# Optimization experiments

Measured on AMD Instinct MI355X. Metric: run time of the kernel, lower is better.

The kernel has to match this reference:

```python
import jax, jax.numpy as jnp
import numpy as np
from jax import lax

FMAP = 64          # feature map H=W
STRIDE = 16
TILE = 16
IMG = 1024         # image H=W (image_shape[1]==image_shape[2])
PRE_NMS = 1000
POST_NMS = 300
NMS_THR = 0.7
RATIOS = np.array([0.5, 1.0, 2.0])
SCALES = np.array([8.0, 16.0, 32.0])


def _make_anchors():
    # meshgrid order (x, y, ratio, scale) with 'ij' indexing, then reshape(-1, 4)
    gx, gy, gr, gs = np.meshgrid(np.arange(FMAP), np.arange(FMAP),
                                 np.arange(len(RATIOS)), np.arange(len(SCALES)),
                                 indexing='ij')
    half_w = 0.5 * TILE * SCALES[gs] * np.sqrt(RATIOS[gr])
    half_h = 0.5 * TILE * SCALES[gs] * np.sqrt(1.0 / RATIOS[gr])
    cx = (gx + 0.5) * STRIDE
    cy = (gy + 0.5) * STRIDE
    z = np.stack([cx - half_w, cy - half_h, cx + half_w, cy + half_h], axis=-1)
    return jnp.asarray(z.reshape(-1, 4).astype(np.float32))  # (H*W*A, 4)


def setup_inputs() -> dict:
    key = jax.random.key(0)
    ks = jax.random.split(key, 6)
    B, Cin, F, A = 8, 256, 256, 9
    inputs = jax.random.normal(ks[0], (B, Cin, FMAP, FMAP), jnp.float32)
    bboxes = jax.random.uniform(ks[1], (B, 16, 4), jnp.float32) * IMG  # unused in inference path
    w_conv = jax.random.normal(ks[2], (F, Cin, 3, 3), jnp.float32) * 0.02
    b_conv = jnp.zeros((F,), jnp.float32)
    w_clf = jax.random.normal(ks[3], (2 * A, F, 1, 1), jnp.float32) * 0.02
    b_clf = jnp.zeros((2 * A,), jnp.float32)
    w_reg = jax.random.normal(ks[4], (4 * A, F, 1, 1), jnp.float32) * 0.02
    b_reg = jnp.zeros((4 * A,), jnp.float32)
    anchors = _make_anchors()
    return {"inputs": inputs, "bboxes": bboxes, "anchors": anchors,
            "w_conv": w_conv, "b_conv": b_conv,
            "w_clf": w_clf, "b_clf": b_clf,
            "w_reg": w_reg, "b_reg": b_reg}


def _conv(x, w, b):
    y = lax.conv_general_dilated(x, w, (1, 1), 'SAME',
                                 dimension_numbers=('NCHW', 'OIHW', 'NCHW'))
    return y + b[None, :, None, None]


def _nms_rois(boxes, batch_idx):
    # boxes: (PRE_NMS, 4), sorted by score descending. Greedy NMS.
    n = boxes.shape[0]
    lb = jnp.maximum(boxes[:, None, :2], boxes[None, :, :2])
    ub = jnp.minimum(boxes[:, None, 2:], boxes[None, :, 2:])
    inter = jnp.prod(jnp.clip(ub - lb, 0.0), axis=-1)              # (n, n)
    area = jnp.prod(boxes[:, 2:] - boxes[:, :2], axis=-1)          # (n,)
    iou = inter / (area[:, None] + area[None, :] - inter)
    idxs = jnp.arange(n)

    def body(i, keep):
        sup = (iou[i] > NMS_THR) & keep[i] & (idxs > i)
        return keep & ~sup

    keep = lax.fori_loop(0, n, body, jnp.ones((n,), bool))
    # compact kept boxes (in score order) into the first slots; OOB scatter drops
    pos = jnp.where(keep, jnp.cumsum(keep) - 1, n + POST_NMS)
    rois = jnp.zeros((POST_NMS, 5), boxes.dtype).at[:, 0].set(batch_idx.astype(boxes.dtype))
    rois = rois.at[pos, 1:].set(boxes, mode='drop')
    return rois


def reference(inputs, bboxes, anchors, w_conv, b_conv, w_clf, b_clf, w_reg, b_reg):
    B, _, H, W = inputs.shape
    x = jax.nn.relu(_conv(inputs, w_conv, b_conv))                  # (B, F, H, W)
    clf = _conv(x, w_clf, b_clf)                                    # (B, 2A, H, W)
    A = clf.shape[1] // 2
    prob = jax.nn.softmax(clf.reshape(B, 2, A, H, W), axis=1)
    scores = prob[:, 1].transpose(0, 2, 3, 1).reshape(B, -1)        # (B, H*W*A)
    reg = _conv(x, w_reg, b_reg).transpose(0, 2, 3, 1).reshape(B, -1, 4)
    # decode anchors with deltas
    sizes = anchors[:, 2:] - anchors[:, :2]                          # (N, 2)
    centers = 0.5 * (anchors[:, 2:] + anchors[:, :2])
    pred_centers = reg[..., :2] * sizes + centers
    pred_sizes = jnp.exp(reg[..., 2:]) * sizes
    props = jnp.concatenate([pred_centers - 0.5 * pred_sizes,
                             pred_centers + 0.5 * pred_sizes], axis=-1)
    lim = jnp.asarray([IMG - 1, IMG - 1, IMG - 1, IMG - 1], props.dtype)
    props = jnp.clip(props, 0.0, lim)
    # pre-NMS top-k by score
    _, top_idx = lax.top_k(scores, PRE_NMS)
    top_props = jnp.take_along_axis(props, top_idx[..., None], axis=1)  # (B, PRE, 4)
    rois = jax.vmap(_nms_rois)(top_props, jnp.arange(B))            # (B, POST, 5)
    return rois
```

## Files before the change

### kernel.cpp

```cpp
#include <hip/hip_runtime.h>

typedef unsigned long long ULL;
typedef double v4d __attribute__((ext_vector_type(4)));


__device__ __forceinline__ ULL fkey64(double f) {
    ULL u = (ULL)__double_as_longlong(f);
    return (u & 0x8000000000000000ull) ? ~u : (u | 0x8000000000000000ull);
}

__global__ void prep_all(const float* __restrict__ wconv,
                         const float* __restrict__ wclf, const float* __restrict__ bclf,
                         double* __restrict__ wmf,
                         double* __restrict__ wdiff, double* __restrict__ bdiff) {
    int blk = blockIdx.x;
    if (blk < 2304) {
        int e = blk * 256 + threadIdx.x;
        int co = e & 63;
        int r = e >> 6;
        int cil = r & 3;
        int r2 = r >> 2;
        int tap = r2 % 9;
        int r3 = r2 / 9;
        int cg = r3 & 3;
        int cc = r3 >> 2;
        int ci = cc * 4 + cil;
        int gco = cg * 64 + co;
        wmf[e] = (double)wconv[(gco * 256 + ci) * 9 + tap];
    } else {
        int a = blk - 2304;
        int c = threadIdx.x;
        wdiff[a * 256 + c] = (double)wclf[(9 + a) * 256 + c] - (double)wclf[a * 256 + c];
        if (c == 0) bdiff[a] = (double)bclf[9 + a] - (double)bclf[a];
    }
}

__global__ __launch_bounds__(256)
__attribute__((amdgpu_waves_per_eu(4, 4)))
void conv3x3_mfma_f64(
    const float* __restrict__ xin, const double* __restrict__ wmf,
    const float* __restrict__ bias, double* __restrict__ y)
{
    __shared__ double wlds[2304];
    __shared__ float  xs[864];

    const int t = threadIdx.x;
    const int blk = blockIdx.x;
    const int b = blk >> 8;
    const int h = (blk >> 2) & 63;
    const int cg = blk & 3;
    const int lane = t & 63;
    const int wid = t >> 6;
    const int arow = lane & 15;
    const int kq = lane >> 4;

    int x_ld[4], x_go[4];
#pragma unroll
    for (int i = 0; i < 4; i++) {
        int e = t + i * 256;
        x_ld[i] = -1; x_go[i] = -1;
        if (e < 792) {
            int cil = e / 198; int rem = e - cil * 198;
            int row = rem / 66; int c = rem - row * 66;
            int hh = h - 1 + row; int col = c - 1;
            x_ld[i] = cil * 216 + row * 72 + c;
            if (hh >= 0 && hh < 64 && col >= 0 && col < 64)
                x_go[i] = cil * 4096 + hh * 64 + col;
        }
    }

    const float* xb = xin + (size_t)b * 1048576;
    const double* wsrc = wmf + (size_t)cg * 2304;

    v4d pz = {0.0, 0.0, 0.0, 0.0};
    v4d prow = __builtin_amdgcn_mfma_f64_16x16x4f64((double)arow, 1.0, pz, 0, 0, 0);
    v4d pcol = __builtin_amdgcn_mfma_f64_16x16x4f64(1.0, (double)arow, pz, 0, 0, 0);
    int rmap[4], cmap[4];
#pragma unroll
    for (int g = 0; g < 4; g++) {
        rmap[g] = (int)(prow[g] * 0.25 + 0.5);
        cmap[g] = (int)(pcol[g] * 0.25 + 0.5);
    }

    float xreg[4];
    double wreg[9];
#pragma unroll
    for (int i = 0; i < 4; i++)
        xreg[i] = (x_ld[i] >= 0 && x_go[i] >= 0) ? xb[x_go[i]] : 0.f;
#pragma unroll
    for (int i = 0; i < 9; i++) wreg[i] = wsrc[t + i * 256];

    v4d acc[4];
#pragma unroll
    for (int nt = 0; nt < 4; nt++) acc[nt] = (v4d){0.0, 0.0, 0.0, 0.0};

    for (int cc = 0; cc < 64; ++cc) {
        __syncthreads();
#pragma unroll
        for (int i = 0; i < 4; i++) if (x_ld[i] >= 0) xs[x_ld[i]] = xreg[i];
#pragma unroll
        for (int i = 0; i < 9; i++) wlds[t + i * 256] = wreg[i];
        __syncthreads();

        if (cc < 63) {
#pragma unroll
            for (int i = 0; i < 4; i++)
                xreg[i] = (x_ld[i] >= 0 && x_go[i] >= 0) ? xb[(cc + 1) * 16384 + x_go[i]] : 0.f;
#pragma unroll
            for (int i = 0; i < 9; i++) wreg[i] = wsrc[(size_t)(cc + 1) * 9216 + t + i * 256];
        }

        const float* xsp = xs + kq * 216 + wid * 16 + arow;
        const double* wsp = wlds + kq * 64 + arow;
#pragma unroll
        for (int kh = 0; kh < 3; kh++) {
#pragma unroll
            for (int kw = 0; kw < 3; kw++) {
                const int tap = kh * 3 + kw;
                double a = (double)xsp[kh * 72 + kw];
#pragma unroll
                for (int nt = 0; nt < 4; nt++)
                    acc[nt] = __builtin_amdgcn_mfma_f64_16x16x4f64(
                        a, wsp[tap * 256 + nt * 16], acc[nt], 0, 0, 0);
            }
        }
    }

    const size_t pixbase = (size_t)(b * 4096 + h * 64 + wid * 16);
#pragma unroll
    for (int nt = 0; nt < 4; nt++) {
#pragma unroll
        for (int g = 0; g < 4; g++) {
            int co = cg * 64 + nt * 16 + cmap[g];
            double v = fmax(acc[nt][g] + (double)bias[co], 0.0);
            y[(pixbase + rmap[g]) * 256 + co] = v;
        }
    }
}

__global__ __launch_bounds__(256) void head_clf2w(
    const double* __restrict__ y, const double* __restrict__ wdiff,
    const double* __restrict__ bdiff, double* __restrict__ dlog)
{
    const int px = blockIdx.x * 4 + (threadIdx.x >> 6);
    const int lane = threadIdx.x & 63;

    const double* yr = y + (size_t)px * 256;
    double yv[4];
#pragma unroll
    for (int k = 0; k < 4; k++) yv[k] = yr[lane + k * 64];

    double s[9];
#pragma unroll
    for (int a = 0; a < 9; a++) {
        const double* wr = wdiff + a * 256;
        double v = 0.0;
#pragma unroll
        for (int k = 0; k < 4; k++) v = fma(wr[lane + k * 64], yv[k], v);
        s[a] = v;
    }
#pragma unroll
    for (int off = 32; off > 0; off >>= 1) {
#pragma unroll
        for (int a = 0; a < 9; a++) s[a] += __shfl_xor(s[a], off);
    }
    if (lane < 9) dlog[(size_t)px * 9 + lane] = s[lane] + bdiff[lane];
}

__global__ __launch_bounds__(1024, 1) void topk1000(
    const double* __restrict__ dlog, int* __restrict__ selidx)
{
    const int b = blockIdx.x;
    const int t = threadIdx.x;
    const double* d = dlog + (size_t)b * 36864;

    ULL key[36];
#pragma unroll
    for (int j = 0; j < 36; j++) key[j] = fkey64(d[t + j * 1024]);

    __shared__ unsigned int hist[2048];
    __shared__ ULL sh_prefix;
    __shared__ unsigned int sh_need;
    const int rep = (t >> 6) & 7;

    ULL prefix = 0ull;
    int need = 1000;
    for (int rs = 56; rs >= 0; rs -= 8) {
        hist[t] = 0u; hist[t + 1024] = 0u;
        __syncthreads();
        ULL mhi = (rs == 56) ? 0ull : (~0ull << (rs + 8));
#pragma unroll
        for (int j = 0; j < 36; j++) {
            ULL u = key[j];
            if ((u & mhi) == prefix)
                atomicAdd(&hist[rep * 256 + ((unsigned int)(u >> rs) & 255u)], 1u);
        }
        __syncthreads();
        if (t < 64) {
            unsigned int c[4];
#pragma unroll
            for (int j = 0; j < 4; j++) {
                unsigned int s = 0u;
#pragma unroll
                for (int rr = 0; rr < 8; rr++) s += hist[rr * 256 + 4 * t + j];
                c[j] = s;
            }
            const unsigned int s4 = c[0] + c[1] + c[2] + c[3];
            unsigned int S = s4;
#pragma unroll
            for (int off = 1; off < 64; off <<= 1) {
                unsigned int o = __shfl_down(S, off);
                if (t + off < 64) S += o;
            }
            ULL m = __ballot(S >= (unsigned int)need);
            int lstar = 63 - __builtin_clzll(m);
            if (t == lstar) {
                const unsigned int T = S - s4;
                const unsigned int nd = (unsigned int)need;
                int vs; unsigned int ca;
                if (T + c[3] >= nd)                    { vs = 4 * t + 3; ca = T; }
                else if (T + c[3] + c[2] >= nd)        { vs = 4 * t + 2; ca = T + c[3]; }
                else if (T + c[3] + c[2] + c[1] >= nd) { vs = 4 * t + 1; ca = T + c[3] + c[2]; }
                else                    { vs = 4 * t;     ca = T + c[3] + c[2] + c[1]; }
                sh_prefix = prefix | ((ULL)vs << rs);
                sh_need = nd - ca;
            }
        }
        __syncthreads();
        prefix = sh_prefix;
        need = (int)sh_need;
    }

    const ULL K = prefix;
    const int count_above = 1000 - need;
    __shared__ ULL skey[1024];
    __shared__ int sidx[1024];
    __shared__ unsigned int cgt, ceq;
    if (t == 0) { cgt = 0u; ceq = 0u; }
    skey[t] = ~0ull;
    sidx[t] = 0x7FFFFFFF;
    __syncthreads();
#pragma unroll
    for (int j = 0; j < 36; j++) {
        ULL u = key[j];
        int i = t + j * 1024;
        if (u > K) {
            unsigned int s = atomicAdd(&cgt, 1u);
            skey[s] = ~u; sidx[s] = i;
        } else if (u == K) {
            unsigned int s = atomicAdd(&ceq, 1u) + (unsigned int)count_above;
            if (s < 1024u) { skey[s] = ~u; sidx[s] = i; }
        }
    }
    __syncthreads();
    for (int k = 2; k <= 1024; k <<= 1) {
        for (int j = k >> 1; j > 0; j >>= 1) {
            int ixj = t ^ j;
            if (ixj > t) {
                ULL ka = skey[t], kb = skey[ixj];
                int ia = sidx[t], ib = sidx[ixj];
                bool up = ((t & k) == 0);
                bool gt = (ka > kb) || (ka == kb && ia > ib);
                bool lt = (ka < kb) || (ka == kb && ia < ib);
                if (up ? gt : lt) {
                    skey[t] = kb; skey[ixj] = ka;
                    sidx[t] = ib; sidx[ixj] = ia;
                }
            }
            __syncthreads();
        }
    }
    if (t < 1000) selidx[b * 1000 + t] = sidx[t];
}

__global__ __launch_bounds__(256) void decode_boxes2(
    const double* __restrict__ y, const int* __restrict__ selidx,
    const float* __restrict__ wregp, const float* __restrict__ bregp,
    const float* __restrict__ anchors, double4* __restrict__ boxes)
{
    const int roi  = (blockIdx.x * 256 + threadIdx.x) >> 6;
    const int lane = threadIdx.x & 63;
    const int b = roi / 1000;
    const int n = selidx[roi];
    const int a = n % 9;
    const int pix = n / 9;

    const double2* yrow = (const double2*)(y + ((size_t)(b * 4096 + pix)) * 256);
    double2 ya = yrow[lane];
    double2 yc = yrow[lane + 64];

    double s[4];
#pragma unroll
    for (int c = 0; c < 4; c++) {
        const float* wp = wregp + (4 * a + c) * 256;
        float2 wa = *(const float2*)(wp + 2 * lane);
        float2 wc = *(const float2*)(wp + 128 + 2 * lane);
        double v = 0.0;
        v = fma((double)wa.x, ya.x, v);
        v = fma((double)wa.y, ya.y, v);
        v = fma((double)wc.x, yc.x, v);
        v = fma((double)wc.y, yc.y, v);
        s[c] = v;
    }
#pragma unroll
    for (int off = 32; off > 0; off >>= 1) {
#pragma unroll
        for (int c = 0; c < 4; c++) s[c] += __shfl_xor(s[c], off);
    }

    if (lane == 0) {
        double a0 = s[0] + (double)bregp[4 * a + 0];
        double a1 = s[1] + (double)bregp[4 * a + 1];
        double a2 = s[2] + (double)bregp[4 * a + 2];
        double a3 = s[3] + (double)bregp[4 * a + 3];
        float4 an = ((const float4*)anchors)[n];
        double ax1 = an.x, ay1 = an.y, ax2 = an.z, ay2 = an.w;
        double aw = ax2 - ax1, ah = ay2 - ay1;
        double cx = 0.5 * (ax1 + ax2), cy = 0.5 * (ay1 + ay2);
        double pcx = a0 * aw + cx, pcy = a1 * ah + cy;
        double pw = exp(a2) * aw, ph = exp(a3) * ah;
        double x1b = pcx - 0.5 * pw, y1b = pcy - 0.5 * ph;
        double x2b = pcx + 0.5 * pw, y2b = pcy + 0.5 * ph;
        x1b = fmin(fmax(x1b, 0.0), 1023.0);
        y1b = fmin(fmax(y1b, 0.0), 1023.0);
        x2b = fmin(fmax(x2b, 0.0), 1023.0);
        y2b = fmin(fmax(y2b, 0.0), 1023.0);
        double4 o; o.x = x1b; o.y = y1b; o.z = x2b; o.w = y2b;
        boxes[roi] = o;
    }
}

__global__ __launch_bounds__(1024) void nms_mask_k(
    const double4* __restrict__ boxes, ULL* __restrict__ mask)
{
    int b = blockIdx.x >> 3;
    int sub = blockIdx.x & 7;
    __shared__ double4 bx[1000];
    for (int i = threadIdx.x; i < 1000; i += 1024) bx[i] = boxes[b * 1000 + i];
    __syncthreads();
    for (int ml = threadIdx.x; ml < 2000; ml += 1024) {
        int m = sub * 2000 + ml;
        int i = m >> 4;
        int wc = m & 15;
        ULL bits = 0ull;
        int j0 = wc << 6;
        if (j0 + 63 > i) {
            double4 bi = bx[i];
            double ai = (bi.z - bi.x) * (bi.w - bi.y);
            int js = max(j0, i + 1);
            int je = min(j0 + 64, 1000);
            for (int j = js; j < je; j++) {
                double4 bj = bx[j];
                double lx = fmax(bi.x, bj.x), ly = fmax(bi.y, bj.y);
                double ux = fmin(bi.z, bj.z), uy = fmin(bi.w, bj.w);
                double iw = fmax(ux - lx, 0.0), ih = fmax(uy - ly, 0.0);
                double inter = iw * ih;
                double aj = (bj.z - bj.x) * (bj.w - bj.y);
                double iou = inter / (ai + aj - inter);
                if (iou > 0.7) bits |= (1ull << (j - j0));
            }
        }
        mask[(size_t)b * 16000 + m] = bits;
    }
}

__global__ __launch_bounds__(1024) void nms_scan_k(
    const ULL* __restrict__ mask, const double4* __restrict__ boxes,
    float* __restrict__ out)
{
    int b = blockIdx.x;
    int t = threadIdx.x;
    __shared__ ULL smask[16000];
    __shared__ ULL keepw[16];
    {
        const ULL* mrow = mask + (size_t)b * 16000;
        for (int i = t; i < 16000; i += 1024) smask[i] = mrow[i];
    }
    __syncthreads();
    if (t < 64) {
        int lane = t;
        ULL remv = 0ull, cur = 0ull;
        ULL pf[16];
#pragma unroll
        for (int q = 0; q < 16; q++) pf[q] = (lane < 16) ? smask[q * 16 + lane] : 0ull;
        for (int base = 0; base < 1000; base += 16) {
#pragma unroll
            for (int q = 0; q < 16; q++) {
                int i = base + q;
                if (i < 1000) {
                    ULL m = pf[q];
                    int c = i >> 6;
                    ULL mc = __shfl(m, c);
                    bool rem = ((cur >> (i & 63)) & 1ull) != 0ull;
                    if (!rem) { remv |= m; cur |= mc; }
                    if (((i + 1) & 63) == 0) cur = __shfl(remv, (i + 1) >> 6);
                    int nx = i + 16;
                    pf[q] = (lane < 16 && nx < 1000) ? smask[nx * 16 + lane] : 0ull;
                }
            }
        }
        if (lane < 16) keepw[lane] = ~remv;
    }
    __syncthreads();
    if (t < 300) {
        float* row = out + (size_t)(b * 300 + t) * 5;
        row[0] = (float)b; row[1] = 0.f; row[2] = 0.f; row[3] = 0.f; row[4] = 0.f;
    }
    __syncthreads();
    if (t < 1000) {
        ULL kw = keepw[t >> 6];
        if ((kw >> (t & 63)) & 1ull) {
            int pos = (int)__popcll(kw & ((1ull << (t & 63)) - 1ull));
            for (int w = 0; w < (t >> 6); w++) pos += (int)__popcll(keepw[w]);
            if (pos < 300) {
                double4 bv = boxes[b * 1000 + t];
                float* row = out + (size_t)(b * 300 + pos) * 5;
                row[1] = (float)bv.x; row[2] = (float)bv.y;
                row[3] = (float)bv.z; row[4] = (float)bv.w;
            }
        }
    }
}

extern "C" void kernel_launch(void* const* d_in, const int* in_sizes, int n_in,
                              void* d_out, int out_size, void* d_ws, size_t ws_size,
                              hipStream_t stream)
{
    const float* xin     = (const float*)d_in[0];
    const float* anchors = (const float*)d_in[2];
    const float* wconv   = (const float*)d_in[3];
    const float* bconv   = (const float*)d_in[4];
    const float* wclf    = (const float*)d_in[5];
    const float* bclf    = (const float*)d_in[6];
    const float* wregp   = (const float*)d_in[7];
    const float* bregp   = (const float*)d_in[8];
    float* out = (float*)d_out;

    char* base = (char*)d_ws;
    double*  y      = (double*)(base);
    double*  wmf    = (double*)(base + 67108864);
    double4* boxes  = (double4*)(base + 67108864);
    ULL*     mask   = (ULL*)(base + 67364864);
    int*     selidx = (int*)(base + 68388864);
    double*  dlog   = (double*)(base + 71827456);
    double*  wdiff  = (double*)(base + 74186752);
    double*  bdiff  = (double*)(base + 74205184);

    prep_all<<<2313, 256, 0, stream>>>(wconv, wclf, bclf, wmf, wdiff, bdiff);
    conv3x3_mfma_f64<<<2048, 256, 0, stream>>>(xin, wmf, bconv, y);
    head_clf2w<<<8192, 256, 0, stream>>>(y, wdiff, bdiff, dlog);
    topk1000<<<8, 1024, 0, stream>>>(dlog, selidx);
    decode_boxes2<<<2000, 256, 0, stream>>>(y, selidx, wregp, bregp, anchors, boxes);
    nms_mask_k<<<64, 1024, 0, stream>>>(boxes, mask);
    nms_scan_k<<<8, 1024, 0, stream>>>(mask, boxes, out);
}
```

Baseline: 955.6 us.

## Compute two output rows per block in FP64 MFMA conv to reuse weights

Each conv block now computes two adjacent output rows instead of one. It loads a 4-row input halo and reuses each weight fragment read from LDS for two MFMAs, and the grid is halved. This cuts weight global and LDS traffic per output and the number of barriers per unit of work. In exchange it doubles accumulator registers, which may hurt occupancy under the fixed waves-per-EU hint, and it leaves fewer blocks to fill the GPU.

```diff
diff --git a/kernel.cpp b/kernel.cpp
--- a/kernel.cpp
+++ b/kernel.cpp
@@ -42,28 +42,29 @@
     const float* __restrict__ bias, double* __restrict__ y)
 {
     __shared__ double wlds[2304];
-    __shared__ float  xs[864];
+    __shared__ float  xs[1152];
 
     const int t = threadIdx.x;
     const int blk = blockIdx.x;
-    const int b = blk >> 8;
-    const int h = (blk >> 2) & 63;
+    const int b = blk >> 7;
+    const int rp = (blk >> 2) & 31;
     const int cg = blk & 3;
+    const int h0 = rp * 2;
     const int lane = t & 63;
     const int wid = t >> 6;
     const int arow = lane & 15;
     const int kq = lane >> 4;
 
-    int x_ld[4], x_go[4];
-#pragma unroll
-    for (int i = 0; i < 4; i++) {
+    int x_ld[5], x_go[5];
+#pragma unroll
+    for (int i = 0; i < 5; i++) {
         int e = t + i * 256;
         x_ld[i] = -1; x_go[i] = -1;
-        if (e < 792) {
-            int cil = e / 198; int rem = e - cil * 198;
+        if (e < 1056) {
+            int cil = e / 264; int rem = e - cil * 264;
             int row = rem / 66; int c = rem - row * 66;
-            int hh = h - 1 + row; int col = c - 1;
-            x_ld[i] = cil * 216 + row * 72 + c;
+            int hh = h0 - 1 + row; int col = c - 1;
+            x_ld[i] = cil * 288 + row * 72 + c;
             if (hh >= 0 && hh < 64 && col >= 0 && col < 64)
                 x_go[i] = cil * 4096 + hh * 64 + col;
         }
@@ -82,58 +83,65 @@
         cmap[g] = (int)(pcol[g] * 0.25 + 0.5);
     }
 
-    float xreg[4];
+    float xreg[5];
     double wreg[9];
 #pragma unroll
-    for (int i = 0; i < 4; i++)
+    for (int i = 0; i < 5; i++)
         xreg[i] = (x_ld[i] >= 0 && x_go[i] >= 0) ? xb[x_go[i]] : 0.f;
 #pragma unroll
     for (int i = 0; i < 9; i++) wreg[i] = wsrc[t + i * 256];
 
-    v4d acc[4];
-#pragma unroll
-    for (int nt = 0; nt < 4; nt++) acc[nt] = (v4d){0.0, 0.0, 0.0, 0.0};
+    v4d acc0[4], acc1[4];
+#pragma unroll
+    for (int nt = 0; nt < 4; nt++) {
+        acc0[nt] = (v4d){0.0, 0.0, 0.0, 0.0};
+        acc1[nt] = (v4d){0.0, 0.0, 0.0, 0.0};
+    }
 
     for (int cc = 0; cc < 64; ++cc) {
         __syncthreads();
 #pragma unroll
-        for (int i = 0; i < 4; i++) if (x_ld[i] >= 0) xs[x_ld[i]] = xreg[i];
+        for (int i = 0; i < 5; i++) if (x_ld[i] >= 0) xs[x_ld[i]] = xreg[i];
 #pragma unroll
         for (int i = 0; i < 9; i++) wlds[t + i * 256] = wreg[i];
         __syncthreads();
 
         if (cc < 63) {
 #pragma unroll
-            for (int i = 0; i < 4; i++)
+            for (int i = 0; i < 5; i++)
                 xreg[i] = (x_ld[i] >= 0 && x_go[i] >= 0) ? xb[(cc + 1) * 16384 + x_go[i]] : 0.f;
 #pragma unroll
             for (int i = 0; i < 9; i++) wreg[i] = wsrc[(size_t)(cc + 1) * 9216 + t + i * 256];
         }
 
-        const float* xsp = xs + kq * 216 + wid * 16 + arow;
+        const float* xsp = xs + kq * 288 + wid * 16 + arow;
         const double* wsp = wlds + kq * 64 + arow;
 #pragma unroll
         for (int kh = 0; kh < 3; kh++) {
 #pragma unroll
             for (int kw = 0; kw < 3; kw++) {
                 const int tap = kh * 3 + kw;
-                double a = (double)xsp[kh * 72 + kw];
-#pragma unroll
-                for (int nt = 0; nt < 4; nt++)
-                    acc[nt] = __builtin_amdgcn_mfma_f64_16x16x4f64(
-                        a, wsp[tap * 256 + nt * 16], acc[nt], 0, 0, 0);
-            }
-        }
-    }
-
-    const size_t pixbase = (size_t)(b * 4096 + h * 64 + wid * 16);
+                double a0 = (double)xsp[kh * 72 + kw];
+                double a1 = (double)xsp[(kh + 1) * 72 + kw];
+#pragma unroll
+                for (int nt = 0; nt < 4; nt++) {
+                    double bf = wsp[tap * 256 + nt * 16];
+                    acc0[nt] = __builtin_amdgcn_mfma_f64_16x16x4f64(a0, bf, acc0[nt], 0, 0, 0);
+                    acc1[nt] = __builtin_amdgcn_mfma_f64_16x16x4f64(a1, bf, acc1[nt], 0, 0, 0);
+                }
+            }
+        }
+    }
+
+    const size_t pix0 = (size_t)(b * 4096 + h0 * 64 + wid * 16);
 #pragma unroll
     for (int nt = 0; nt < 4; nt++) {
 #pragma unroll
         for (int g = 0; g < 4; g++) {
             int co = cg * 64 + nt * 16 + cmap[g];
-            double v = fmax(acc[nt][g] + (double)bias[co], 0.0);
-            y[(pixbase + rmap[g]) * 256 + co] = v;
+            double bv = (double)bias[co];
+            y[(pix0 + rmap[g]) * 256 + co]      = fmax(acc0[nt][g] + bv, 0.0);
+            y[(pix0 + 64 + rmap[g]) * 256 + co] = fmax(acc1[nt][g] + bv, 0.0);
         }
     }
 }
@@ -447,7 +455,7 @@
     double*  bdiff  = (double*)(base + 74205184);
 
     prep_all<<<2313, 256, 0, stream>>>(wconv, wclf, bclf, wmf, wdiff, bdiff);
-    conv3x3_mfma_f64<<<2048, 256, 0, stream>>>(xin, wmf, bconv, y);
+    conv3x3_mfma_f64<<<1024, 256, 0, stream>>>(xin, wmf, bconv, y);
     head_clf2w<<<8192, 256, 0, stream>>>(y, wdiff, bdiff, dlog);
     topk1000<<<8, 1024, 0, stream>>>(dlog, selidx);
     decode_boxes2<<<2000, 256, 0, stream>>>(y, selidx, wregp, bregp, anchors, boxes);
```

Result: faster. 936.7 us, median of 2 (-2.0%).
